# Kernel optimization log

Measured on AMD Instinct MI355X. Metric: run time of the kernel, lower is better.

## Reference

```python
import jax, jax.numpy as jnp
import numpy as np
import math

NUM_HEADS = 16
HEAD_DIM = 128
ROPE_BASE = 10000.0


def setup_inputs() -> dict:
    key = jax.random.key(0)
    ks = jax.random.split(key, 6)
    B, S, H = 2, 2048, 2048
    hidden_states = jax.random.normal(ks[0], (B, S, H), dtype=jnp.float32) * 0.02
    # causal additive mask, shape (B, 1, S, S)
    neg = jnp.finfo(jnp.float32).min
    causal = jnp.where(jnp.tril(jnp.ones((S, S), dtype=bool)), 0.0, neg).astype(jnp.float32)
    attention_mask = jnp.broadcast_to(causal[None, None], (B, 1, S, S))
    position_ids = jnp.broadcast_to(jnp.arange(S, dtype=jnp.int64)[None], (B, S))
    scale = 1.0 / math.sqrt(H)
    Wq = jax.random.normal(ks[1], (H, H), dtype=jnp.float32) * scale
    Wk = jax.random.normal(ks[2], (H, H), dtype=jnp.float32) * scale
    Wv = jax.random.normal(ks[3], (H, H), dtype=jnp.float32) * scale
    Wo = jax.random.normal(ks[4], (H, H), dtype=jnp.float32) * scale
    return {"hidden_states": hidden_states, "attention_mask": attention_mask,
            "position_ids": position_ids, "Wq": Wq, "Wk": Wk, "Wv": Wv, "Wo": Wo}


def _rotate_half(x):
    x1, x2 = jnp.split(x, 2, axis=-1)
    return jnp.concatenate((-x2, x1), axis=-1)


def reference(hidden_states, attention_mask, position_ids, Wq, Wk, Wv, Wo):
    B, S, H = hidden_states.shape
    nh, hd = NUM_HEADS, HEAD_DIM

    def shape_heads(x):  # (B,S,H) -> (B,nh,S,hd)
        return x.reshape(B, S, nh, hd).transpose(0, 2, 1, 3)

    q = shape_heads(hidden_states @ Wq.T)
    k = shape_heads(hidden_states @ Wk.T)
    v = shape_heads(hidden_states @ Wv.T)

    kv_seq_len = S  # no past_key_value
    # rotary table: (kv_seq_len, hd)
    inv_freq = 1.0 / (ROPE_BASE ** (jnp.arange(0, hd, 2, dtype=jnp.float32) / hd))
    t = jnp.arange(kv_seq_len, dtype=jnp.float32)
    freqs = jnp.einsum('i,j->ij', t, inv_freq)
    emb = jnp.concatenate((freqs, freqs), axis=-1)
    # gather-based RoPE == table lookup at position_ids: (B,S,hd) -> (B,1,S,hd)
    cos = jnp.cos(emb)[position_ids][:, None]
    sin = jnp.sin(emb)[position_ids][:, None]

    q = q * cos + _rotate_half(q) * sin
    k = k * cos + _rotate_half(k) * sin

    scores = jnp.einsum('bhqd,bhkd->bhqk', q, k) / math.sqrt(hd)
    scores = scores + attention_mask
    scores = jnp.maximum(scores, jnp.finfo(scores.dtype).min)
    probs = jax.nn.softmax(scores.astype(jnp.float32), axis=-1).astype(q.dtype)
    attn = jnp.einsum('bhqk,bhkd->bhqd', probs, v)  # (B,nh,S,hd)
    attn = attn.transpose(0, 2, 1, 3).reshape(B, S, H)
    return attn @ Wo.T
```

## Files before the change

### kernel.cpp

```cpp
#include <hip/hip_runtime.h>
#include <hip/hip_bf16.h>
#include <cstdint>

#define SQ    2048
#define HDIM  2048
#define NH    16
#define HD    128
#define BATCH 2
#define MTOK  (BATCH*SQ)

typedef unsigned short u16;
typedef unsigned int   u32;
typedef __bf16 bf16x8 __attribute__((ext_vector_type(8)));
typedef float  f32x4  __attribute__((ext_vector_type(4)));
typedef float  f32x16 __attribute__((ext_vector_type(16)));
typedef unsigned short u16x4 __attribute__((ext_vector_type(4)));
typedef unsigned int   u32x4 __attribute__((ext_vector_type(4)));

__device__ __forceinline__ u16 f2b(float f) {
  union { float f; unsigned u; } v; v.f = f;
  return (u16)((v.u + 0x7fffu + ((v.u >> 16) & 1u)) >> 16);
}
__device__ __forceinline__ float b2f(u16 b) {
  union { unsigned u; float f; } v; v.u = ((unsigned)b) << 16;
  return v.f;
}

#define GLD_LDS16(gp, lp) __builtin_amdgcn_global_load_lds( \
    (const __attribute__((address_space(1))) uint32_t*)(gp), \
    (__attribute__((address_space(3))) uint32_t*)(lp), 16, 0, 0)

__device__ __forceinline__ f32x16 zero16() {
  f32x16 v;
#pragma unroll
  for (int i = 0; i < 16; ++i) v[i] = 0.f;
  return v;
}

__global__ __launch_bounds__(256) void conv_bf16(const float* __restrict__ in,
                                                 u16* __restrict__ out, int n4) {
  int i = blockIdx.x * 256 + threadIdx.x;
  if (i >= n4) return;
  float4 v = ((const float4*)in)[i];
  u16x4 o;
  o.x = f2b(v.x); o.y = f2b(v.y); o.z = f2b(v.z); o.w = f2b(v.w);
  *(u16x4*)(out + (size_t)i * 4) = o;
}

__global__ __launch_bounds__(256) void conv_w4(const float* __restrict__ w0,
                                               const float* __restrict__ w1,
                                               const float* __restrict__ w2,
                                               const float* __restrict__ w3,
                                               u16* o0, u16* o1, u16* o2, u16* o3) {
  int i = blockIdx.x * 256 + threadIdx.x;
  int sel = blockIdx.y;
  const float* in = sel == 0 ? w0 : sel == 1 ? w1 : sel == 2 ? w2 : w3;
  u16* out = sel == 0 ? o0 : sel == 1 ? o1 : sel == 2 ? o2 : o3;
  float4 v = ((const float4*)in)[i];
  u16x4 o;
  o.x = f2b(v.x); o.y = f2b(v.y); o.z = f2b(v.z); o.w = f2b(v.w);
  *(u16x4*)(out + (size_t)i * 4) = o;
}

__global__ __launch_bounds__(256) void addk(const float* __restrict__ a,
                                            const float* __restrict__ b,
                                            float* __restrict__ o) {
  int i = blockIdx.x * 256 + threadIdx.x;
  float4 x = ((const float4*)a)[i], y = ((const float4*)b)[i];
  float4 r; r.x = x.x + y.x; r.y = x.y + y.y; r.z = x.z + y.z; r.w = x.w + y.w;
  ((float4*)o)[i] = r;
}

__global__ void rope_table_k(float* __restrict__ ct, float* __restrict__ st) {
  int s = blockIdx.x, j = threadIdx.x;
  float invf = expf(-(float)j * (9.210340371976184f / 64.0f));
  float ang = (float)s * invf;
  ct[s * 64 + j] = cosf(ang);
  st[s * 64 + j] = sinf(ang);
}

template<int OUT>
__global__ __launch_bounds__(512, 1)
void gemm8m(const u16* __restrict__ A, const u16* __restrict__ W0,
            const u16* __restrict__ W1, const u16* __restrict__ W2,
            u16* __restrict__ oQ, u16* __restrict__ oK, u16* __restrict__ oV,
            float* __restrict__ oF, float* __restrict__ oF2,
            const float* __restrict__ ct, const float* __restrict__ st,
            int nt) {
  __shared__ char smem[131072];
  u16 (*Ah)[2][128 * 64] = (u16(*)[2][128 * 64])smem;
  u16 (*Bh)[2][128 * 64] = (u16(*)[2][128 * 64])(smem + 65536);
  const int tid = threadIdx.x, lane = tid & 63, w = tid >> 6;
  const int wm = w >> 2, wn = w & 3;
  const int gx = gridDim.x;
  const int lin = blockIdx.y * gx + blockIdx.x;
  const int cpx = (gx * gridDim.y) >> 3;
  const int swz = (lin & 7) * cpx + (lin >> 3);
  const int bx = swz % gx, by = swz / gx;
  const int m0 = by * 256;
  const int n0g = bx * 256;
  const int kbase = (OUT == 1) ? (int)blockIdx.z * 1024 : 0;
  int sel; const u16* Bw; int nloc;
  if (OUT == 0) {
    sel = n0g >> 11;
    Bw = (sel == 0) ? W0 : (sel == 1) ? W1 : W2;
    nloc = n0g & 2047;
  } else {
    sel = 0; Bw = W0; nloc = n0g;
  }
  float* dstF = (OUT == 1) ? (blockIdx.z ? oF2 : oF) : oF;

  u32 aoff[2][2], boff[2][2];
#pragma unroll
  for (int h = 0; h < 2; ++h) {
#pragma unroll
    for (int l = 0; l < 2; ++l) {
      int c = l * 512 + tid, ra = c >> 3, sl = c & 7;
      int r = ((ra >> 6) << 7) + h * 64 + (ra & 63);
      aoff[h][l] = (u32)((m0 + r) * HDIM + kbase + ((sl ^ (ra & 7)) * 8));
      int col = nloc + ((ra >> 5) * 64) + h * 32 + (ra & 31);
      boff[h][l] = (u32)(col * HDIM + kbase + ((sl ^ (ra & 7)) * 8));
    }
  }
  auto stageA = [&](int buf, int h, int k0) {
#pragma unroll
    for (int l = 0; l < 2; ++l)
      GLD_LDS16(A + (size_t)aoff[h][l] + k0, &Ah[buf][h][(l * 512 + tid) * 8]);
  };
  auto stageB = [&](int buf, int h, int k0) {
#pragma unroll
    for (int l = 0; l < 2; ++l)
      GLD_LDS16(Bw + (size_t)boff[h][l] + k0, &Bh[buf][h][(l * 512 + tid) * 8]);
  };

  f32x4 acc[8][4];
#pragma unroll
  for (int i = 0; i < 8; ++i)
#pragma unroll
    for (int j = 0; j < 4; ++j) acc[i][j] = (f32x4){0.f, 0.f, 0.f, 0.f};

  const int l15 = lane & 15, hi4 = lane >> 4;
  const int swr = (l15 & 7) << 4;

  bf16x8 afv0[4][2], afv1[4][2];
  bf16x8 bfv0[2][2], bfv1[2][2];

  auto readA = [&](bf16x8 (&dst)[4][2], const char* Ab) {
#pragma unroll
    for (int j = 0; j < 4; ++j)
#pragma unroll
      for (int kk = 0; kk < 2; ++kk)
        dst[j][kk] = *(const bf16x8*)(Ab + (wm * 64 + j * 16 + l15) * 128 +
                                      ((kk * 64 + hi4 * 16) ^ swr));
  };
  auto readB = [&](bf16x8 (&dst)[2][2], const char* Bb) {
#pragma unroll
    for (int j2 = 0; j2 < 2; ++j2)
#pragma unroll
      for (int kk = 0; kk < 2; ++kk)
        dst[j2][kk] = *(const bf16x8*)(Bb + (wn * 32 + j2 * 16 + l15) * 128 +
                                       ((kk * 64 + hi4 * 16) ^ swr));
  };
  auto mfq = [&](bf16x8 (&af)[4][2], bf16x8 (&bf)[2][2], int mh, int nh) {
#pragma unroll
    for (int kk = 0; kk < 2; ++kk)
#pragma unroll
      for (int j = 0; j < 4; ++j)
#pragma unroll
        for (int j2 = 0; j2 < 2; ++j2)
          acc[mh * 4 + j][nh * 2 + j2] = __builtin_amdgcn_mfma_f32_16x16x32_bf16(
              af[j][kk], bf[j2][kk], acc[mh * 4 + j][nh * 2 + j2], 0, 0, 0);
  };

  stageA(0, 0, 0); stageB(0, 0, 0); stageA(0, 1, 0); stageB(0, 1, 0);
  asm volatile("s_waitcnt vmcnt(4)" ::: "memory");
  __builtin_amdgcn_s_barrier();

  for (int t = 0; t < nt; ++t) {
    const int cur = t & 1, nb = cur ^ 1;
    const bool st2 = (t + 1 < nt);
    const int kn = (t + 1) * 64;
    const char* Ab0 = (const char*)&Ah[cur][0][0];
    const char* Ab1 = (const char*)&Ah[cur][1][0];
    const char* Bb0 = (const char*)&Bh[cur][0][0];
    const char* Bb1 = (const char*)&Bh[cur][1][0];

    readA(afv0, Ab0); readB(bfv0, Bb0);
    if (st2) {
      stageA(nb, 0, kn); stageB(nb, 0, kn);
      asm volatile("s_waitcnt vmcnt(6)" ::: "memory");
    } else {
      asm volatile("s_waitcnt vmcnt(2)" ::: "memory");
    }
    __builtin_amdgcn_s_barrier();
    asm volatile("s_waitcnt lgkmcnt(0)" ::: "memory");
    __builtin_amdgcn_sched_barrier(0);
    __builtin_amdgcn_s_setprio(1); mfq(afv0, bfv0, 0, 0); __builtin_amdgcn_s_setprio(0);

    readA(afv1, Ab1);
    if (st2) {
      stageA(nb, 1, kn);
      asm volatile("s_waitcnt vmcnt(6)" ::: "memory");
    } else {
      asm volatile("s_waitcnt vmcnt(0)" ::: "memory");
    }
    __builtin_amdgcn_s_barrier();
    asm volatile("s_waitcnt lgkmcnt(0)" ::: "memory");
    __builtin_amdgcn_sched_barrier(0);
    __builtin_amdgcn_s_setprio(1); mfq(afv1, bfv0, 1, 0); __builtin_amdgcn_s_setprio(0);

    readB(bfv1, Bb1);
    if (st2) stageB(nb, 1, kn);
    __builtin_amdgcn_s_barrier();
    asm volatile("s_waitcnt lgkmcnt(0)" ::: "memory");
    __builtin_amdgcn_sched_barrier(0);
    __builtin_amdgcn_s_setprio(1); mfq(afv0, bfv1, 0, 1); __builtin_amdgcn_s_setprio(0);

    if (st2) asm volatile("s_waitcnt vmcnt(4)" ::: "memory");
    __builtin_amdgcn_s_barrier();
    __builtin_amdgcn_s_setprio(1); mfq(afv1, bfv1, 1, 1); __builtin_amdgcn_s_setprio(0);
  }

  const int cl = l15, rg = hi4 * 4;
  if (OUT == 0 && sel != 2) {
    float* Ls = (float*)smem;
    u16* O = sel ? oK : oQ;
#pragma unroll
    for (int mh = 0; mh < 2; ++mh) {
      __builtin_amdgcn_s_barrier();
      if (wm == mh) {
#pragma unroll
        for (int mi = 0; mi < 8; ++mi)
#pragma unroll
          for (int ni = 0; ni < 4; ++ni) {
            const int n = wn * 64 + ni * 16 + cl;
#pragma unroll
            for (int r = 0; r < 4; ++r) {
              const int lrow = mi * 16 + rg + r;
              Ls[lrow * 256 + (n ^ (((lrow >> 2) & 3) << 4))] = acc[mi][ni][r];
            }
          }
      }
      __builtin_amdgcn_s_barrier();
      if (wm == mh) {
#pragma unroll
        for (int mi = 0; mi < 8; ++mi)
#pragma unroll
          for (int ni = 0; ni < 4; ++ni) {
            const int n = wn * 64 + ni * 16 + cl;
            const int ng = nloc + n, h = ng >> 7, d = ng & 127, j = d & 63;
#pragma unroll
            for (int r = 0; r < 4; ++r) {
              const int lrow = mi * 16 + rg + r;
              const int m = m0 + mh * 128 + lrow;
              const int b = m >> 11, s = m & (SQ - 1);
              float x  = acc[mi][ni][r];
              float xo = Ls[lrow * 256 + ((n ^ 64) ^ (((lrow >> 2) & 3) << 4))];
              float c = ct[s * 64 + j], sn = st[s * 64 + j];
              float res = (d < 64) ? (x * c - xo * sn) : (x * c + xo * sn);
              O[((size_t)(b * NH + h) * SQ + s) * HD + d] = f2b(res);
            }
          }
      }
    }
    return;
  }
#pragma unroll
  for (int mi = 0; mi < 8; ++mi) {
#pragma unroll
    for (int ni = 0; ni < 4; ++ni) {
      const int mb = m0 + wm * 128 + mi * 16 + rg;
      const int n = nloc + wn * 64 + ni * 16 + cl;
      if (OUT == 1) {
#pragma unroll
        for (int r = 0; r < 4; ++r)
          dstF[(size_t)(mb + r) * HDIM + n] = acc[mi][ni][r];
      } else {
        const int h = n >> 7, d = n & 127;
        const int b = mb >> 11, s = mb & (SQ - 1);
        u16x4 pk;
        pk.x = f2b(acc[mi][ni][0]); pk.y = f2b(acc[mi][ni][1]);
        pk.z = f2b(acc[mi][ni][2]); pk.w = f2b(acc[mi][ni][3]);
        *(u16x4*)&oV[((size_t)(b * NH + h) * HD + d) * SQ + s] = pk;
      }
    }
  }
}

__device__ __forceinline__ void stage_kv(u16* ksb, u16* vsb,
                                         const u16* __restrict__ Kg,
                                         const u16* __restrict__ Vg,
                                         int kv0, int w, int lane) {
#pragma unroll
  for (int i = 0; i < 4; ++i) {
    int chunk = (w * 4 + i) * 64 + lane;
    int row = chunk >> 4, c16 = chunk & 15;
    int csrc = c16 ^ (row & 15);
    GLD_LDS16(Kg + (size_t)(kv0 + row) * HD + csrc * 8, ksb + (w * 4 + i) * 512);
  }
#pragma unroll
  for (int i = 0; i < 4; ++i) {
    int chunk = (w * 4 + i) * 64 + lane;
    int d = chunk >> 3, c8 = chunk & 7;
    int csrc = c8 ^ (d & 7);
    GLD_LDS16(Vg + (size_t)d * SQ + kv0 + csrc * 8, vsb + (w * 4 + i) * 512);
  }
}

#define MKPA(dst, P, off) { \
  u32 u0_, u1_, u2_, u3_; \
  asm("v_cvt_pk_bf16_f32 %0, %1, %2" : "=v"(u0_) : "v"(P[off + 0]), "v"(P[off + 1])); \
  asm("v_cvt_pk_bf16_f32 %0, %1, %2" : "=v"(u1_) : "v"(P[off + 2]), "v"(P[off + 3])); \
  asm("v_cvt_pk_bf16_f32 %0, %1, %2" : "=v"(u2_) : "v"(P[off + 4]), "v"(P[off + 5])); \
  asm("v_cvt_pk_bf16_f32 %0, %1, %2" : "=v"(u3_) : "v"(P[off + 6]), "v"(P[off + 7])); \
  u32 x0_ = (u32)__shfl_xor((int)u0_, 32, 64); \
  u32 x1_ = (u32)__shfl_xor((int)u1_, 32, 64); \
  u32 x2_ = (u32)__shfl_xor((int)u2_, 32, 64); \
  u32 x3_ = (u32)__shfl_xor((int)u3_, 32, 64); \
  u32x4 w_; \
  w_.x = hi ? x2_ : u0_; \
  w_.y = hi ? x3_ : u1_; \
  w_.z = hi ? u2_ : x0_; \
  w_.w = hi ? u3_ : x1_; \
  dst = __builtin_bit_cast(bf16x8, w_); \
}

#define PVD(oD, dblk) { \
  const int dr_ = (dblk) * 32 + l31; \
  const int sw_ = (dr_ & 7) << 4; \
  bf16x8 v0_ = *(const bf16x8*)(Vb + ((dr_ * 128 +  0 + hi * 16) ^ sw_)); \
  oD = __builtin_amdgcn_mfma_f32_32x32x16_bf16(pa[0], v0_, oD, 0, 0, 0); \
  bf16x8 v1_ = *(const bf16x8*)(Vb + ((dr_ * 128 + 32 + hi * 16) ^ sw_)); \
  oD = __builtin_amdgcn_mfma_f32_32x32x16_bf16(pa[1], v1_, oD, 0, 0, 0); \
  bf16x8 v2_ = *(const bf16x8*)(Vb + ((dr_ * 128 + 64 + hi * 16) ^ sw_)); \
  oD = __builtin_amdgcn_mfma_f32_32x32x16_bf16(pa[2], v2_, oD, 0, 0, 0); \
  bf16x8 v3_ = *(const bf16x8*)(Vb + ((dr_ * 128 + 96 + hi * 16) ^ sw_)); \
  oD = __builtin_amdgcn_mfma_f32_32x32x16_bf16(pa[3], v3_, oD, 0, 0, 0); \
}

__global__ __launch_bounds__(256, 2)
void flash_fwd2(const u16* __restrict__ Q, const u16* __restrict__ K,
                const u16* __restrict__ Vt, u16* __restrict__ Out) {
  __shared__ u16 Ks[2][64 * 128];
  __shared__ u16 Vs[2][128 * 64];
  const int tid = threadIdx.x, lane = tid & 63, w = tid >> 6;
  const int hi = lane >> 5, l31 = lane & 31;
  const int qt = 15 - (int)(blockIdx.x >> 5);
  const int bh = blockIdx.x & 31;
  const int q0 = qt * 128;
  const u16* Qg = Q + (size_t)bh * SQ * HD;
  const u16* Kg = K + (size_t)bh * SQ * HD;
  const u16* Vg = Vt + (size_t)bh * HD * SQ;
  const int qw = q0 + w * 32;
  const int qg = qw + l31;

  bf16x8 qf[8];
#pragma unroll
  for (int st = 0; st < 8; ++st)
    qf[st] = *(const bf16x8*)&Qg[(size_t)qg * HD + st * 16 + hi * 8];

  f32x16 o0 = zero16(), o1 = zero16(), o2 = zero16(), o3 = zero16();
  float lsum = 0.f;
  const float sL2E = 0.1275174446f;
  const int ktl = 2 * qt + 1;
  int cur = 0;

  stage_kv(Ks[0], Vs[0], Kg, Vg, 0, w, lane);

  for (int kt = 0; kt <= ktl; ++kt) {
    if (kt < ktl) {
      stage_kv(Ks[cur ^ 1], Vs[cur ^ 1], Kg, Vg, (kt + 1) * 64, w, lane);
      asm volatile("s_waitcnt vmcnt(8)" ::: "memory");
    } else {
      asm volatile("s_waitcnt vmcnt(0)" ::: "memory");
    }
    __builtin_amdgcn_s_barrier();

    const int kv0 = kt * 64;
    if (kv0 <= qw + 31) {
      const char* Kb = (const char*)Ks[cur];
      const char* Vb = (const char*)Vs[cur];
      f32x16 c0 = zero16(), c1 = zero16();
      const int kr0 = l31, kr1 = 32 + l31;
      const int sw0 = (l31 & 15) << 4;
#pragma unroll
      for (int st = 0; st < 8; ++st) {
        bf16x8 k0 = *(const bf16x8*)(Kb + ((kr0 * 256 + st * 32 + hi * 16) ^ sw0));
        c0 = __builtin_amdgcn_mfma_f32_32x32x16_bf16(k0, qf[st], c0, 0, 0, 0);
        bf16x8 k1 = *(const bf16x8*)(Kb + ((kr1 * 256 + st * 32 + hi * 16) ^ sw0));
        c1 = __builtin_amdgcn_mfma_f32_32x32x16_bf16(k1, qf[st], c1, 0, 0, 0);
      }
      const bool needmask = (kv0 + 63 > qw);
      const int lim0 = qg - kv0, lim1 = lim0 - 32;
      if (needmask) {
#pragma unroll
        for (int r = 0; r < 16; ++r) {
          const int cr = (r & 3) + 8 * (r >> 2) + 4 * hi;
          float p0 = exp2f(c0[r] * sL2E);
          c0[r] = (cr <= lim0) ? p0 : 0.f;
          float p1 = exp2f(c1[r] * sL2E);
          c1[r] = (cr <= lim1) ? p1 : 0.f;
          lsum += c0[r] + c1[r];
        }
      } else {
#pragma unroll
        for (int r = 0; r < 16; ++r) {
          c0[r] = exp2f(c0[r] * sL2E);
          c1[r] = exp2f(c1[r] * sL2E);
          lsum += c0[r] + c1[r];
        }
      }
      bf16x8 pa[4];
      MKPA(pa[0], c0, 0); MKPA(pa[1], c0, 8);
      MKPA(pa[2], c1, 0); MKPA(pa[3], c1, 8);
      PVD(o0, 0) PVD(o1, 1) PVD(o2, 2) PVD(o3, 3)
    }
    __builtin_amdgcn_s_barrier();
    cur ^= 1;
  }

  float ltot = lsum + __shfl_xor(lsum, 32, 64);
  float invl = 1.f / ltot;
  const int b = bh >> 4, h = bh & 15;
#pragma unroll
  for (int g = 0; g < 4; ++g) {
#pragma unroll
    for (int j = 0; j < 4; ++j) {
      const int r = g * 4 + j;
      const int cr = g * 8 + 4 * hi + j;
      float inv = __shfl(invl, cr, 64);
      const int s = q0 + w * 32 + cr;
      size_t rb = ((size_t)(b * SQ + s)) * HDIM + h * HD;
      Out[rb +  0 + l31] = f2b(o0[r] * inv);
      Out[rb + 32 + l31] = f2b(o1[r] * inv);
      Out[rb + 64 + l31] = f2b(o2[r] * inv);
      Out[rb + 96 + l31] = f2b(o3[r] * inv);
    }
  }
}

extern "C" void kernel_launch(void* const* d_in, const int* in_sizes, int n_in,
                              void* d_out, int out_size, void* d_ws, size_t ws_size,
                              hipStream_t stream) {
  const float* hs = (const float*)d_in[0];
  const float* Wq = (const float*)d_in[3];
  const float* Wk = (const float*)d_in[4];
  const float* Wv = (const float*)d_in[5];
  const float* Wo = (const float*)d_in[6];

  char* ws = (char*)d_ws;
  u16* XB  = (u16*)(ws);
  u16* WQB = (u16*)(ws + (size_t)(16 << 20));
  u16* WKB = (u16*)(ws + (size_t)(24 << 20));
  u16* WVB = (u16*)(ws + (size_t)(32 << 20));
  u16* WOB = (u16*)(ws + (size_t)(40 << 20));
  u16* QR  = (u16*)(ws + (size_t)(48 << 20));
  u16* KR  = (u16*)(ws + (size_t)(64 << 20));
  u16* VT  = (u16*)(ws + (size_t)(80 << 20));
  u16* ATT = (u16*)(ws + (size_t)(96 << 20));
  float* CT = (float*)(ws + (size_t)(112 << 20));
  float* ST = (float*)(ws + (size_t)(112 << 20) + (1 << 19));
  float* P0 = (float*)(ws);
  float* P1 = (float*)(ws + (size_t)(48 << 20));

  conv_bf16<<<8192, 256, 0, stream>>>(hs, XB, 2097152);
  conv_w4<<<dim3(4096, 4), 256, 0, stream>>>(Wq, Wk, Wv, Wo, WQB, WKB, WVB, WOB);
  rope_table_k<<<SQ, 64, 0, stream>>>(CT, ST);

  gemm8m<0><<<dim3(24, 16), 512, 0, stream>>>(XB, WQB, WKB, WVB,
                                              QR, KR, VT, nullptr, nullptr,
                                              CT, ST, 32);

  flash_fwd2<<<512, 256, 0, stream>>>(QR, KR, VT, ATT);

  gemm8m<1><<<dim3(8, 16, 2), 512, 0, stream>>>(ATT, WOB, nullptr, nullptr,
                                                nullptr, nullptr, nullptr,
                                                P0, P1, nullptr, nullptr, 16);
  addk<<<8192, 256, 0, stream>>>(P0, P1, (float*)d_out);
}
```

Before: 270.1 us.

## Deepen GEMM prefetch to two K-tiles ahead with unrolled double-buffer loop

Restructures the bf16 GEMM main loop into a two-iteration unroll that prefetches two K tiles ahead into both shared-memory buffers, with static buffer pointers and revised vmcnt/lgkmcnt waits. Each buffer is refilled only after a barrier confirms all waves have finished reading it. The goal is to hide more global-load latency behind MFMA work. The cost is many extra barriers per iteration, and the loop assumes nt is even, which holds for 32 and 16.

Result: slower. 277.8 us (+2.9%).

```diff
diff --git a/kernel.cpp b/kernel.cpp
--- a/kernel.cpp
+++ b/kernel.cpp
@@ -81,7 +81,7 @@
 
 template<int OUT>
 __global__ __launch_bounds__(512, 1)
-void gemm8m(const u16* __restrict__ A, const u16* __restrict__ W0,
+void gemm8p(const u16* __restrict__ A, const u16* __restrict__ W0,
             const u16* __restrict__ W1, const u16* __restrict__ W2,
             u16* __restrict__ oQ, u16* __restrict__ oK, u16* __restrict__ oV,
             float* __restrict__ oF, float* __restrict__ oF2,
@@ -173,52 +173,89 @@
   };
 
   stageA(0, 0, 0); stageB(0, 0, 0); stageA(0, 1, 0); stageB(0, 1, 0);
-  asm volatile("s_waitcnt vmcnt(4)" ::: "memory");
+  stageA(1, 0, 64); stageB(1, 0, 64); stageA(1, 1, 64); stageB(1, 1, 64);
+  asm volatile("s_waitcnt vmcnt(8)" ::: "memory");
   __builtin_amdgcn_s_barrier();
 
-  for (int t = 0; t < nt; ++t) {
-    const int cur = t & 1, nb = cur ^ 1;
-    const bool st2 = (t + 1 < nt);
-    const int kn = (t + 1) * 64;
-    const char* Ab0 = (const char*)&Ah[cur][0][0];
-    const char* Ab1 = (const char*)&Ah[cur][1][0];
-    const char* Bb0 = (const char*)&Bh[cur][0][0];
-    const char* Bb1 = (const char*)&Bh[cur][1][0];
-
-    readA(afv0, Ab0); readB(bfv0, Bb0);
-    if (st2) {
-      stageA(nb, 0, kn); stageB(nb, 0, kn);
-      asm volatile("s_waitcnt vmcnt(6)" ::: "memory");
-    } else {
-      asm volatile("s_waitcnt vmcnt(2)" ::: "memory");
-    }
+  const char* A00 = (const char*)&Ah[0][0][0];
+  const char* A01 = (const char*)&Ah[0][1][0];
+  const char* B00 = (const char*)&Bh[0][0][0];
+  const char* B01 = (const char*)&Bh[0][1][0];
+  const char* A10 = (const char*)&Ah[1][0][0];
+  const char* A11 = (const char*)&Ah[1][1][0];
+  const char* B10 = (const char*)&Bh[1][0][0];
+  const char* B11 = (const char*)&Bh[1][1][0];
+
+  for (int it = 0; it < nt / 2; ++it) {
+    const int t = it * 2;
+    const bool pre = (t + 2 < nt);
+    const int k2 = (t + 2) * 64, k3 = (t + 3) * 64;
+
+    readA(afv0, A00); readB(bfv0, B00);
+    asm volatile("s_waitcnt lgkmcnt(8)" ::: "memory");
     __builtin_amdgcn_s_barrier();
     asm volatile("s_waitcnt lgkmcnt(0)" ::: "memory");
     __builtin_amdgcn_sched_barrier(0);
     __builtin_amdgcn_s_setprio(1); mfq(afv0, bfv0, 0, 0); __builtin_amdgcn_s_setprio(0);
-
-    readA(afv1, Ab1);
-    if (st2) {
-      stageA(nb, 1, kn);
-      asm volatile("s_waitcnt vmcnt(6)" ::: "memory");
-    } else {
-      asm volatile("s_waitcnt vmcnt(0)" ::: "memory");
-    }
+    __builtin_amdgcn_s_barrier();
+
+    readA(afv1, A01);
+    if (pre) { stageA(0, 0, k2); stageB(0, 0, k2); }
     __builtin_amdgcn_s_barrier();
     asm volatile("s_waitcnt lgkmcnt(0)" ::: "memory");
     __builtin_amdgcn_sched_barrier(0);
     __builtin_amdgcn_s_setprio(1); mfq(afv1, bfv0, 1, 0); __builtin_amdgcn_s_setprio(0);
-
-    readB(bfv1, Bb1);
-    if (st2) stageB(nb, 1, kn);
+    __builtin_amdgcn_s_barrier();
+
+    readB(bfv1, B01);
+    if (pre) stageA(0, 1, k2);
     __builtin_amdgcn_s_barrier();
     asm volatile("s_waitcnt lgkmcnt(0)" ::: "memory");
     __builtin_amdgcn_sched_barrier(0);
     __builtin_amdgcn_s_setprio(1); mfq(afv0, bfv1, 0, 1); __builtin_amdgcn_s_setprio(0);
-
-    if (st2) asm volatile("s_waitcnt vmcnt(4)" ::: "memory");
+    __builtin_amdgcn_s_barrier();
+
+    if (pre) {
+      stageB(0, 1, k2);
+      asm volatile("s_waitcnt vmcnt(8)" ::: "memory");
+    } else {
+      asm volatile("s_waitcnt vmcnt(0)" ::: "memory");
+    }
     __builtin_amdgcn_s_barrier();
     __builtin_amdgcn_s_setprio(1); mfq(afv1, bfv1, 1, 1); __builtin_amdgcn_s_setprio(0);
+    __builtin_amdgcn_s_barrier();
+
+    readA(afv0, A10); readB(bfv0, B10);
+    asm volatile("s_waitcnt lgkmcnt(8)" ::: "memory");
+    __builtin_amdgcn_s_barrier();
+    asm volatile("s_waitcnt lgkmcnt(0)" ::: "memory");
+    __builtin_amdgcn_sched_barrier(0);
+    __builtin_amdgcn_s_setprio(1); mfq(afv0, bfv0, 0, 0); __builtin_amdgcn_s_setprio(0);
+    __builtin_amdgcn_s_barrier();
+
+    readA(afv1, A11);
+    if (pre) { stageA(1, 0, k3); stageB(1, 0, k3); }
+    __builtin_amdgcn_s_barrier();
+    asm volatile("s_waitcnt lgkmcnt(0)" ::: "memory");
+    __builtin_amdgcn_sched_barrier(0);
+    __builtin_amdgcn_s_setprio(1); mfq(afv1, bfv0, 1, 0); __builtin_amdgcn_s_setprio(0);
+    __builtin_amdgcn_s_barrier();
+
+    readB(bfv1, B11);
+    if (pre) stageA(1, 1, k3);
+    __builtin_amdgcn_s_barrier();
+    asm volatile("s_waitcnt lgkmcnt(0)" ::: "memory");
+    __builtin_amdgcn_sched_barrier(0);
+    __builtin_amdgcn_s_setprio(1); mfq(afv0, bfv1, 0, 1); __builtin_amdgcn_s_setprio(0);
+    __builtin_amdgcn_s_barrier();
+
+    if (pre) {
+      stageB(1, 1, k3);
+      asm volatile("s_waitcnt vmcnt(8)" ::: "memory");
+    }
+    __builtin_amdgcn_s_barrier();
+    __builtin_amdgcn_s_setprio(1); mfq(afv1, bfv1, 1, 1); __builtin_amdgcn_s_setprio(0);
+    __builtin_amdgcn_s_barrier();
   }
 
   const int cl = l15, rg = hi4 * 4;
@@ -467,13 +504,13 @@
   conv_w4<<<dim3(4096, 4), 256, 0, stream>>>(Wq, Wk, Wv, Wo, WQB, WKB, WVB, WOB);
   rope_table_k<<<SQ, 64, 0, stream>>>(CT, ST);
 
-  gemm8m<0><<<dim3(24, 16), 512, 0, stream>>>(XB, WQB, WKB, WVB,
+  gemm8p<0><<<dim3(24, 16), 512, 0, stream>>>(XB, WQB, WKB, WVB,
                                               QR, KR, VT, nullptr, nullptr,
                                               CT, ST, 32);
 
   flash_fwd2<<<512, 256, 0, stream>>>(QR, KR, VT, ATT);
 
-  gemm8m<1><<<dim3(8, 16, 2), 512, 0, stream>>>(ATT, WOB, nullptr, nullptr,
+  gemm8p<1><<<dim3(8, 16, 2), 512, 0, stream>>>(ATT, WOB, nullptr, nullptr,
                                                 nullptr, nullptr, nullptr,
                                                 P0, P1, nullptr, nullptr, 16);
   addk<<<8192, 256, 0, stream>>>(P0, P1, (float*)d_out);
```
